# Kernel optimization log

Hardware: AMD Instinct MI355X
Metric: run time of the kernel (lower is better)

## Reference

```python
import jax, jax.numpy as jnp
import numpy as np

EPS = 1e-12
H = 256
W = 256
RANK = 4
CTX = 1024
BATCH = 32
FF = (H + W) * RANK * 4  # 8192
STD = 0.001


def _norm(x, axis):
    # torch: (x - mean) / sqrt(var(unbiased) + eps)
    m = jnp.mean(x, axis=axis, keepdims=True)
    v = jnp.var(x, axis=axis, keepdims=True, ddof=1)
    return (x - m) / jnp.sqrt(v + EPS)


def _norm_polar(x):
    # x: [B, N, 2]; magnitude-normalize relative to per-batch max magnitude
    x_abs = jnp.sqrt(x[..., 0] ** 2 + x[..., 1] ** 2 + EPS)          # [B, N]
    h = x_abs / (jnp.max(x_abs, axis=-1, keepdims=True) + EPS)       # [B, N]
    xn = x / (x_abs[..., None] + EPS)                                # [B, N, 2]
    return jnp.stack([h * xn[..., 0], h * xn[..., 1]], axis=-1)


def setup_inputs() -> dict:
    key = jax.random.key(0)
    ks = jax.random.split(key, 12)

    def lin(k, fan_in, shape):
        b = 1.0 / np.sqrt(fan_in)
        return jax.random.uniform(k, shape, jnp.float32, -b, b)

    weights_static = jnp.concatenate([
        jax.random.normal(ks[9], (1, H, W, 2), jnp.float32) * STD,
        jax.random.normal(ks[10], (1, H, W, 2), jnp.float32) * STD
        + jnp.array([1.0, 0.0], jnp.float32),
    ], axis=0)  # [2, H, W, 2]

    return {
        "x": jax.random.normal(ks[0], (BATCH, CTX), jnp.float32),
        "W_in": lin(ks[1], CTX, (FF, CTX)),
        "b_in": lin(ks[2], CTX, (FF,)),
        "W_gate": lin(ks[3], CTX, (FF, CTX)),
        "b_gate": lin(ks[4], CTX, (FF,)),
        "W_t": lin(ks[5], FF, (FF, FF)),
        "b_t": lin(ks[6], FF, (FF,)),
        "conv_w": lin(ks[7], RANK, (RANK, RANK)),  # 1x1 conv kernel [out, in]
        "conv_b": lin(ks[8], RANK, (RANK,)),
        "weights_static": weights_static,
        "weights_mod": jax.random.normal(ks[11], (4, H, W), jnp.float32) * STD,
    }


def reference(x, W_in, b_in, W_gate, b_gate, W_t, b_t, conv_w, conv_b,
              weights_static, weights_mod):
    b = x.shape[0]
    # dual linear projections (dropout p=0 -> identity)
    xt = x @ W_in.T + b_in            # [B, FF]
    xg = x @ W_gate.T + b_gate        # [B, FF]
    stack = jnp.stack([xt, xg], axis=0).reshape(2, b, 4, -1)
    stack = _norm(stack, -1)
    ctx = (stack[0] * jnp.tanh(stack[1])).reshape(b, -1)   # gated, [B, FF]
    ctx = ctx @ W_t.T + b_t                                 # [B, FF]
    ctx = ctx.reshape(b, 4, RANK, H + W)
    modc = _norm(ctx, -1)
    # outer product -> [B, 4, RANK, H, W]
    mod = jnp.tanh(jnp.einsum('bkri,bkrj->bkrij', modc[..., :H], modc[..., H:]))
    # channel 0: 1x1 conv over rank channels, then sum channels (keepdim)
    mod_real = jnp.einsum('oi,bihw->bohw', conv_w, mod[:, 0]) + conv_b[None, :, None, None]
    mod_real = jnp.sum(mod_real, axis=1, keepdims=True)     # [B, 1, H, W]
    mod_other = jnp.sum(mod[:, 1:], axis=2)                 # [B, 3, H, W]
    mod = jnp.concatenate([mod_real, mod_other], axis=1)    # [B, 4, H, W]
    mod = weights_mod[None] * mod

    A0 = weights_static[0]            # [H, W, 2]
    A1 = weights_static[1]            # [H, W, 2]
    Bm = jnp.moveaxis(mod[:, 0:2], 1, -1)                   # [B, H, W, 2]
    ms_r = A1[..., 0] * Bm[..., 0] - A1[..., 1] * Bm[..., 1]
    ms_i = A1[..., 0] * Bm[..., 1] - A1[..., 1] * Bm[..., 0]
    mod_scaled = jnp.stack([ms_r, ms_i], axis=-1)           # [B, H, W, 2]
    mod_scaled = _norm_polar(mod_scaled.reshape(b, H * W, 2)).reshape(b, H, W, 2)

    mag = jnp.sqrt(mod_scaled[..., 0] ** 2 + mod_scaled[..., 1] ** 2 + EPS)
    mag = jnp.sqrt(jnp.mean(mag, axis=(-1, -2)) + EPS)      # [B]
    mod_scaled = mod_scaled / mag[:, None, None, None]

    mod_weights = A0[None] + mod_scaled                     # [B, H, W, 2]

    mod_proj = jnp.moveaxis(mod[:, 2:], 1, -1)              # [B, H, W, 2]
    mod_proj = _norm_polar(mod_proj.reshape(b, H * W, 2)).reshape(b, H, W, 2)
    den = jnp.sqrt(mod_proj[..., 0] ** 2 + mod_proj[..., 1] ** 2 + EPS)
    theta_cos = mod_proj[..., 0] / den
    theta_sin = mod_proj[..., 1] / den
    weights = mod_weights[..., 0] * theta_cos + mod_weights[..., 1] * theta_sin
    return weights  # [B, H, W]
```

## Files before the change

### kernel.cpp

```cpp
#include <hip/hip_runtime.h>
#include <cstddef>

#define NB   32
#define CTXD 1024
#define FFD  8192
#define HD   256
#define WD   256
#define NPIX 65536
#define EPSF 1e-12f

typedef __attribute__((ext_vector_type(8))) short bf16x8;
typedef __attribute__((ext_vector_type(4))) float f32x4;


__device__ __forceinline__ float ftanh(float x){
  float ax = fabsf(x);
  float e  = __expf(2.0f*ax);
  float r  = 1.0f - 2.0f*__builtin_amdgcn_rcpf(e + 1.0f);
  return copysignf(r, x);
}

__device__ __forceinline__ unsigned short f2bf(float f){
  unsigned u = __float_as_uint(f);
  unsigned r = (u + 0x7FFFu + ((u >> 16) & 1u)) >> 16;
  return (unsigned short)r;
}
__device__ __forceinline__ float bf2f(unsigned short s){
  return __uint_as_float((unsigned)s << 16);
}

__device__ __forceinline__ void split3(float f, unsigned short& s0,
                                       unsigned short& s1, unsigned short& s2){
  s0 = f2bf(f);
  float r1 = f - bf2f(s0);
  s1 = f2bf(r1);
  float r2 = r1 - bf2f(s1);
  s2 = f2bf(r2);
}

__device__ __forceinline__ void gload_lds16(const void* g, void* l){
  __builtin_amdgcn_global_load_lds(
      (__attribute__((address_space(1))) void*)g,
      (__attribute__((address_space(3))) void*)l, 16, 0, 0);
}

__device__ __forceinline__ void block_reduce4(float& a, float& b, float& c, float& d){
  for (int off = 32; off > 0; off >>= 1){
    a += __shfl_down(a, off); b += __shfl_down(b, off);
    c += __shfl_down(c, off); d += __shfl_down(d, off);
  }
  __shared__ float lds[16];
  int wid = threadIdx.x >> 6, lane = threadIdx.x & 63;
  if (lane == 0){ lds[wid*4+0]=a; lds[wid*4+1]=b; lds[wid*4+2]=c; lds[wid*4+3]=d; }
  __syncthreads();
  a = (lds[0]+lds[4])+(lds[8]+lds[12]);
  b = (lds[1]+lds[5])+(lds[9]+lds[13]);
  c = (lds[2]+lds[6])+(lds[10]+lds[14]);
  d = (lds[3]+lds[7])+(lds[11]+lds[15]);
}

__device__ __forceinline__ void pixel_core(
    const float* __restrict__ lds, int h, int w, int pix,
    float cw0, float cw1, float cw2, float cw3, float cb,
    const float* __restrict__ wmod, const float* __restrict__ wstat,
    float& r_, float& i_, float& p_, float& q_){
  float sk[4];
  #pragma unroll
  for (int k = 0; k < 4; ++k){
    float acc = 0.f;
    #pragma unroll
    for (int r = 0; r < 4; ++r){
      int kr = k*4 + r;
      float u  = lds[kr*512 + h];
      float vv = lds[kr*512 + 256 + w];
      float tt = ftanh(u*vv);
      float cwr = (r==0)?cw0:(r==1)?cw1:(r==2)?cw2:cw3;
      acc += (k==0) ? cwr*tt : tt;
    }
    sk[k] = acc;
  }
  sk[0] += cb;
  float m0 = sk[0]*wmod[0*NPIX+pix];
  float m1 = sk[1]*wmod[1*NPIX+pix];
  float m2 = sk[2]*wmod[2*NPIX+pix];
  float m3 = sk[3]*wmod[3*NPIX+pix];
  float2 A1 = *(const float2*)(wstat + (size_t)(NPIX + pix)*2);
  r_ = A1.x*m0 - A1.y*m1;
  i_ = A1.x*m1 - A1.y*m0;
  p_ = m2; q_ = m3;
}


__global__ __launch_bounds__(256) void k_prep(
    const float* __restrict__ x, unsigned short* __restrict__ P,
    float* __restrict__ red){
  int g = blockIdx.x*256 + threadIdx.x;
  if (g < 64) red[g] = 0.0f;
  int b = g >> 7, grp = g & 127;
  int koff = grp*8;
  int c = grp >> 2, kg = grp & 3;
  const float* src = x + (size_t)b*CTXD + koff;
  float4 v0 = *(const float4*)(src), v1 = *(const float4*)(src+4);
  float vv[8] = {v0.x,v0.y,v0.z,v0.w,v1.x,v1.y,v1.z,v1.w};
  bf16x8 a0, a1, a2;
  #pragma unroll
  for (int e = 0; e < 8; ++e){
    unsigned short s0,s1,s2; split3(vv[e],s0,s1,s2);
    a0[e]=(short)s0; a1[e]=(short)s1; a2[e]=(short)s2;
  }
  size_t base = (size_t)c*3072 + (b>>4)*512 + kg*128 + (b&15)*8;
  *(bf16x8*)(P + base)        = a0;
  *(bf16x8*)(P + base + 1024) = a1;
  *(bf16x8*)(P + base + 2048) = a2;
}

__global__ __launch_bounds__(256) void k_gemm_reuse(
    const float* __restrict__ W0, const float* __restrict__ W1,
    const unsigned short* __restrict__ BP,
    float* __restrict__ Cp, int K, size_t zstride){
  __shared__ float wtile[2][4096];
  __shared__ unsigned short bpack[24576];
  const int t = threadIdx.x;
  const int wv = t >> 6, lane = t & 63;
  const int row = lane & 15, kg = lane >> 4;
  const int f0 = blockIdx.x * 128;
  const int kc = blockIdx.y;
  const float* __restrict__ W = blockIdx.z ? W1 : W0;
  const int kb = kc * 256;

  {
    const unsigned short* bsrc = BP + (size_t)(kc*8)*3072;
    #pragma unroll
    for (int i = 0; i < 12; ++i){
      int call = wv*12 + i;
      gload_lds16(bsrc + call*512 + lane*8, bpack + call*512);
    }
  }
  auto stageW = [&](int buf, int s){
    const int kbase = kb + s*32;
    #pragma unroll
    for (int i = 0; i < 4; ++i){
      int call = wv*4 + i;
      const float* src = W + (size_t)(f0 + call*8 + (lane>>3))*K + kbase
                           + (((lane&7) ^ ((lane>>3)&7)) << 2);
      gload_lds16(src, &wtile[buf][call*256]);
    }
  };

  stageW(0, 0);
  asm volatile("s_waitcnt vmcnt(0)" ::: "memory");
  __syncthreads();

  f32x4 acc0l={0.f,0.f,0.f,0.f}, acc0h={0.f,0.f,0.f,0.f};
  f32x4 acc1l={0.f,0.f,0.f,0.f}, acc1h={0.f,0.f,0.f,0.f};
  int cur = 0;
  const int sw = row & 7;

  for (int s = 0; s < 8; ++s){
    if (s + 1 < 8) stageW(cur ^ 1, s + 1);
    asm volatile("s_waitcnt vmcnt(4)" ::: "memory");
    __builtin_amdgcn_sched_barrier(0);
    const unsigned short* bch = bpack + s*3072 + kg*128 + row*8;
    bf16x8 b0 = *(const bf16x8*)(bch);
    bf16x8 b1 = *(const bf16x8*)(bch +  512);
    bf16x8 b2 = *(const bf16x8*)(bch + 1024);
    bf16x8 b3 = *(const bf16x8*)(bch + 1536);
    bf16x8 b4 = *(const bf16x8*)(bch + 2048);
    bf16x8 b5 = *(const bf16x8*)(bch + 2560);
    #pragma unroll
    for (int T = 0; T < 2; ++T){
      const float* wr = &wtile[cur][(wv*32 + T*16 + row)*32];
      float4 lo = *(const float4*)(wr + (((2*kg  ) ^ sw) << 2));
      float4 hi = *(const float4*)(wr + (((2*kg+1) ^ sw) << 2));
      bf16x8 a0, a1, a2;
      float wv8[8] = {lo.x,lo.y,lo.z,lo.w,hi.x,hi.y,hi.z,hi.w};
      #pragma unroll
      for (int e = 0; e < 8; ++e){
        unsigned short s0,s1,s2; split3(wv8[e],s0,s1,s2);
        a0[e]=(short)s0; a1[e]=(short)s1; a2[e]=(short)s2;
      }
      f32x4 al = T ? acc1l : acc0l, ah = T ? acc1h : acc0h;
      al = __builtin_amdgcn_mfma_f32_16x16x32_bf16(a0, b0, al, 0,0,0);
      ah = __builtin_amdgcn_mfma_f32_16x16x32_bf16(a0, b1, ah, 0,0,0);
      al = __builtin_amdgcn_mfma_f32_16x16x32_bf16(a0, b2, al, 0,0,0);
      ah = __builtin_amdgcn_mfma_f32_16x16x32_bf16(a0, b3, ah, 0,0,0);
      al = __builtin_amdgcn_mfma_f32_16x16x32_bf16(a1, b0, al, 0,0,0);
      ah = __builtin_amdgcn_mfma_f32_16x16x32_bf16(a1, b1, ah, 0,0,0);
      al = __builtin_amdgcn_mfma_f32_16x16x32_bf16(a0, b4, al, 0,0,0);
      ah = __builtin_amdgcn_mfma_f32_16x16x32_bf16(a0, b5, ah, 0,0,0);
      al = __builtin_amdgcn_mfma_f32_16x16x32_bf16(a1, b2, al, 0,0,0);
      ah = __builtin_amdgcn_mfma_f32_16x16x32_bf16(a1, b3, ah, 0,0,0);
      al = __builtin_amdgcn_mfma_f32_16x16x32_bf16(a2, b0, al, 0,0,0);
      ah = __builtin_amdgcn_mfma_f32_16x16x32_bf16(a2, b1, ah, 0,0,0);
      if (T){ acc1l = al; acc1h = ah; } else { acc0l = al; acc0h = ah; }
    }
    cur ^= 1;
  }

  float* __restrict__ C = Cp + (size_t)blockIdx.z*zstride + (size_t)kc*(FFD*32);
  #pragma unroll
  for (int r = 0; r < 4; ++r){
    int fA = f0 + wv*32 + kg*4 + r;
    int fB = fA + 16;
    C[(size_t)fA*32 + row]      = acc0l[r];
    C[(size_t)fA*32 + 16 + row] = acc0h[r];
    C[(size_t)fB*32 + row]      = acc1l[r];
    C[(size_t)fB*32 + 16 + row] = acc1h[r];
  }
}

__global__ __launch_bounds__(256) void k_reduce1(
    const float* __restrict__ Cp, const float* __restrict__ bin,
    const float* __restrict__ bg, float* __restrict__ xtT,
    float* __restrict__ xgT){
  int g = blockIdx.x*256 + threadIdx.x;
  int m = g >> 18, idx = g & 262143;
  int f = idx >> 5;
  const float* __restrict__ cp = Cp + (size_t)m*(4ull*FFD*32);
  float s = (m ? bg : bin)[f];
  #pragma unroll
  for (int sI = 0; sI < 4; ++sI) s += cp[(size_t)sI*(FFD*32) + idx];
  (m ? xgT : xtT)[idx] = s;
}

__global__ __launch_bounds__(256) void k_reduce2(
    const float* __restrict__ Cp, const float* __restrict__ bias,
    float* __restrict__ outT){
  int g = blockIdx.x*256 + threadIdx.x;
  int f = g >> 5;
  float s = bias[f];
  #pragma unroll
  for (int sI = 0; sI < 32; ++sI) s += Cp[(size_t)sI*(FFD*32) + g];
  outT[g] = s;
}

__global__ __launch_bounds__(256) void k_normgate(
    const float* __restrict__ xtT, const float* __restrict__ xgT,
    unsigned short* __restrict__ P){
  int b = blockIdx.x >> 2, g4 = blockIdx.x & 3;
  int t = threadIdx.x;
  int f8 = g4*2048 + t*8;
  float vt[8], vg[8];
  float st=0.f, sst=0.f, sg=0.f, ssg=0.f;
  #pragma unroll
  for (int i = 0; i < 8; ++i){
    int f = f8 + i;
    float a = xtT[(size_t)f*NB + b];
    float c = xgT[(size_t)f*NB + b];
    vt[i]=a; vg[i]=c;
    st += a; sst += a*a; sg += c; ssg += c*c;
  }
  block_reduce4(st, sst, sg, ssg);
  float mt = st * (1.0f/2048.0f);
  float it = rsqrtf((sst - st*mt) * (1.0f/2047.0f) + EPSF);
  float mg = sg * (1.0f/2048.0f);
  float ig = rsqrtf((ssg - sg*mg) * (1.0f/2047.0f) + EPSF);
  bf16x8 a0, a1, a2;
  #pragma unroll
  for (int i = 0; i < 8; ++i){
    float nt = (vt[i]-mt)*it;
    float ng = (vg[i]-mg)*ig;
    float cv = nt * ftanh(ng);
    unsigned short s0,s1,s2; split3(cv,s0,s1,s2);
    a0[i]=(short)s0; a1[i]=(short)s1; a2[i]=(short)s2;
  }
  int c2 = f8 >> 5, kg = (f8 >> 3) & 3;
  size_t base = (size_t)c2*3072 + (b>>4)*512 + kg*128 + (b&15)*8;
  *(bf16x8*)(P + base)        = a0;
  *(bf16x8*)(P + base + 1024) = a1;
  *(bf16x8*)(P + base + 2048) = a2;
}

__global__ __launch_bounds__(256) void k_norm512(
    const float* __restrict__ ctx2T, float* __restrict__ modc){
  int b = blockIdx.x >> 4, kr = blockIdx.x & 15;
  int t = threadIdx.x;
  int base = kr*512;
  float v0 = ctx2T[(base + t      )*NB + b];
  float v1 = ctx2T[(base + 256 + t)*NB + b];
  float s = v0+v1, ss = v0*v0 + v1*v1, d0=0.f, d1=0.f;
  block_reduce4(s, ss, d0, d1);
  float m   = s * (1.0f/512.0f);
  float inv = rsqrtf((ss - s*m) * (1.0f/511.0f) + EPSF);
  modc[b*FFD + base + t      ] = (v0-m)*inv;
  modc[b*FFD + base + 256 + t] = (v1-m)*inv;
}

__global__ __launch_bounds__(256) void k_scan(
    const float* __restrict__ modc,
    const float* __restrict__ convw, const float* __restrict__ convb,
    const float* __restrict__ wmod, const float* __restrict__ wstat,
    float* __restrict__ red, float* __restrict__ magpart){
  int b = blockIdx.x >> 4, chunk = blockIdx.x & 15;
  int t = threadIdx.x;
  __shared__ float lds[16*512];
  #pragma unroll
  for (int i = 0; i < 8; ++i){
    float4 v = *(const float4*)(modc + (size_t)b*FFD + (i*256 + t)*4);
    *(float4*)(lds + (i*256 + t)*4) = v;
  }
  float cw0 = convw[0]+convw[4]+convw[8]+convw[12];
  float cw1 = convw[1]+convw[5]+convw[9]+convw[13];
  float cw2 = convw[2]+convw[6]+convw[10]+convw[14];
  float cw3 = convw[3]+convw[7]+convw[11]+convw[15];
  float cb  = convb[0]+convb[1]+convb[2]+convb[3];
  __syncthreads();
  int w = t;
  float mxs = 0.f, mxp = 0.f, sas = 0.f;
  for (int it = 0; it < 16; ++it){
    int h = chunk*16 + it;
    int pix = h*WD + w;
    float r_, i_, p_, q_;
    pixel_core(lds, h, w, pix, cw0, cw1, cw2, cw3, cb, wmod, wstat,
               r_, i_, p_, q_);
    float as = sqrtf(r_*r_ + i_*i_ + EPSF);
    float ap = sqrtf(p_*p_ + q_*q_ + EPSF);
    mxs = fmaxf(mxs, as); mxp = fmaxf(mxp, ap);
    sas += as;
  }
  for (int off = 32; off > 0; off >>= 1){
    mxs = fmaxf(mxs, __shfl_down(mxs, off));
    mxp = fmaxf(mxp, __shfl_down(mxp, off));
    sas += __shfl_down(sas, off);
  }
  __shared__ float lred[12];
  int wid = t >> 6, lane = t & 63;
  if (lane == 0){ lred[wid] = mxs; lred[4+wid] = mxp; lred[8+wid] = sas; }
  __syncthreads();
  if (t == 0){
    float a = fmaxf(fmaxf(lred[0],lred[1]), fmaxf(lred[2],lred[3]));
    float p = fmaxf(fmaxf(lred[4],lred[5]), fmaxf(lred[6],lred[7]));
    float s = (lred[8]+lred[9])+(lred[10]+lred[11]);
    atomicMax((int*)&red[b],    __float_as_int(a));
    atomicMax((int*)&red[32+b], __float_as_int(p));
    magpart[b*16 + chunk] = s;
  }
}

__global__ __launch_bounds__(256) void k_final(
    const float* __restrict__ modc,
    const float* __restrict__ convw, const float* __restrict__ convb,
    const float* __restrict__ wmod, const float* __restrict__ wstat,
    const float* __restrict__ red, const float* __restrict__ magpart,
    float* __restrict__ out){
  int b = blockIdx.x >> 4, chunk = blockIdx.x & 15;
  int t = threadIdx.x;
  __shared__ float lds[16*512];
  __shared__ float s_im;
  if (t < 16){
    float v = magpart[b*16 + t];
    for (int off = 8; off > 0; off >>= 1) v += __shfl_down(v, off);
    if (t == 0){
      float maxs = red[b];
      s_im = rsqrtf(v*(1.0f/65536.0f)/(maxs + EPSF) + EPSF);
    }
  }
  #pragma unroll
  for (int i = 0; i < 8; ++i){
    float4 v = *(const float4*)(modc + (size_t)b*FFD + (i*256 + t)*4);
    *(float4*)(lds + (i*256 + t)*4) = v;
  }
  float cw0 = convw[0]+convw[4]+convw[8]+convw[12];
  float cw1 = convw[1]+convw[5]+convw[9]+convw[13];
  float cw2 = convw[2]+convw[6]+convw[10]+convw[14];
  float cw3 = convw[3]+convw[7]+convw[11]+convw[15];
  float cb  = convb[0]+convb[1]+convb[2]+convb[3];
  __syncthreads();
  float im = s_im;
  float maxs = red[b], maxp = red[32+b];
  int w = t;
  for (int it = 0; it < 16; ++it){
    int h = chunk*16 + it;
    int pix = h*WD + w;
    float r_, i_, p_, q_;
    pixel_core(lds, h, w, pix, cw0, cw1, cw2, cw3, cb, wmod, wstat,
               r_, i_, p_, q_);
    float as = sqrtf(r_*r_ + i_*i_ + EPSF);
    float fs = (as/(maxs+EPSF))/(as+EPSF)*im;
    float2 A0 = *(const float2*)(wstat + (size_t)pix*2);
    float mwr = A0.x + fs*r_;
    float mwi = A0.y + fs*i_;
    float ap = sqrtf(p_*p_ + q_*q_ + EPSF);
    float fp = (ap/(maxp+EPSF))/(ap+EPSF);
    float mpr = fp*p_, mpi = fp*q_;
    float den = sqrtf(mpr*mpr + mpi*mpi + EPSF);
    out[(size_t)b*NPIX + pix] = (mwr*mpr + mwi*mpi)/den;
  }
}


extern "C" void kernel_launch(void* const* d_in, const int* in_sizes, int n_in,
                              void* d_out, int out_size, void* d_ws, size_t ws_size,
                              hipStream_t stream){
  const float* x     = (const float*)d_in[0];
  const float* Win   = (const float*)d_in[1];
  const float* bin   = (const float*)d_in[2];
  const float* Wg    = (const float*)d_in[3];
  const float* bg    = (const float*)d_in[4];
  const float* Wt    = (const float*)d_in[5];
  const float* bt    = (const float*)d_in[6];
  const float* convw = (const float*)d_in[7];
  const float* convb = (const float*)d_in[8];
  const float* wstat = (const float*)d_in[9];
  const float* wmod  = (const float*)d_in[10];
  float* out = (float*)d_out;
  float* ws  = (float*)d_ws;

  float* xtT   = ws;
  float* xgT   = ws + 262144;
  float* ctx2T = ws;
  float* modc  = ws + 262144;
  unsigned short* P2 = (unsigned short*)(ws + 524288);
  unsigned short* P1 = (unsigned short*)(ws + 917504);
  float* Cp    = ws + 966656;
  float* red     = ws + 9355264;
  float* magpart = ws + 9355328;

  k_prep<<<16, 256, 0, stream>>>(x, P1, red);
  k_gemm_reuse<<<dim3(64,4,2), 256, 0, stream>>>(Win, Wg, P1,
                                                 Cp, CTXD, 4ull*FFD*32);
  k_reduce1<<<2048, 256, 0, stream>>>(Cp, bin, bg, xtT, xgT);
  k_normgate<<<128, 256, 0, stream>>>(xtT, xgT, P2);
  k_gemm_reuse<<<dim3(64,32,1), 256, 0, stream>>>(Wt, Wt, P2,
                                                  Cp, FFD, 0);
  k_reduce2<<<1024, 256, 0, stream>>>(Cp, bt, ctx2T);
  k_norm512<<<512, 256, 0, stream>>>(ctx2T, modc);
  k_scan<<<512, 256, 0, stream>>>(modc, convw, convb, wmod, wstat, red, magpart);
  k_final<<<512, 256, 0, stream>>>(modc, convw, convb, wmod, wstat, red,
                                   magpart, out);
}
```

Before: 160.7 us.

## Use scaled fp16 two-term split MFMA and fuse split-K reductions into norms

Replaces the three-term bf16 splitting of both GEMM operands with a two-term fp16 split, where the residual is scaled by 4096. This cuts the MFMA count per step from 12 to 6 and shrinks the packed B buffer and its LDS footprint. The two accumulator sets are combined at store time. The separate split-K reduction kernels are removed, and the partial sums are added directly inside the normalization kernels, saving two launches and an intermediate round-trip. The risks are lower precision from fp16's narrower range, and strided, uncoalesced partial-sum reads inside the norm kernels.

```diff
diff --git a/kernel.cpp b/kernel.cpp
--- a/kernel.cpp
+++ b/kernel.cpp
@@ -8,8 +8,10 @@
 #define WD   256
 #define NPIX 65536
 #define EPSF 1e-12f
-
-typedef __attribute__((ext_vector_type(8))) short bf16x8;
+#define SCF  4096.0f
+#define ISCF (1.0f/4096.0f)
+
+typedef __attribute__((ext_vector_type(8))) _Float16 half8;
 typedef __attribute__((ext_vector_type(4))) float f32x4;
 
 
@@ -20,22 +22,10 @@
   return copysignf(r, x);
 }
 
-__device__ __forceinline__ unsigned short f2bf(float f){
-  unsigned u = __float_as_uint(f);
-  unsigned r = (u + 0x7FFFu + ((u >> 16) & 1u)) >> 16;
-  return (unsigned short)r;
-}
-__device__ __forceinline__ float bf2f(unsigned short s){
-  return __uint_as_float((unsigned)s << 16);
-}
-
-__device__ __forceinline__ void split3(float f, unsigned short& s0,
-                                       unsigned short& s1, unsigned short& s2){
-  s0 = f2bf(f);
-  float r1 = f - bf2f(s0);
-  s1 = f2bf(r1);
-  float r2 = r1 - bf2f(s1);
-  s2 = f2bf(r2);
+__device__ __forceinline__ void split2h(float f, _Float16& h0, _Float16& h1){
+  h0 = (_Float16)f;
+  float r = (f - (float)h0) * SCF;
+  h1 = (_Float16)r;
 }
 
 __device__ __forceinline__ void gload_lds16(const void* g, void* l){
@@ -97,21 +87,19 @@
   int g = blockIdx.x*256 + threadIdx.x;
   if (g < 64) red[g] = 0.0f;
   int b = g >> 7, grp = g & 127;
-  int koff = grp*8;
   int c = grp >> 2, kg = grp & 3;
-  const float* src = x + (size_t)b*CTXD + koff;
+  const float* src = x + (size_t)b*CTXD + grp*8;
   float4 v0 = *(const float4*)(src), v1 = *(const float4*)(src+4);
   float vv[8] = {v0.x,v0.y,v0.z,v0.w,v1.x,v1.y,v1.z,v1.w};
-  bf16x8 a0, a1, a2;
+  half8 g0, g1;
   #pragma unroll
   for (int e = 0; e < 8; ++e){
-    unsigned short s0,s1,s2; split3(vv[e],s0,s1,s2);
-    a0[e]=(short)s0; a1[e]=(short)s1; a2[e]=(short)s2;
-  }
-  size_t base = (size_t)c*3072 + (b>>4)*512 + kg*128 + (b&15)*8;
-  *(bf16x8*)(P + base)        = a0;
-  *(bf16x8*)(P + base + 1024) = a1;
-  *(bf16x8*)(P + base + 2048) = a2;
+    _Float16 h0,h1; split2h(vv[e],h0,h1);
+    g0[e]=h0; g1[e]=h1;
+  }
+  size_t base = (size_t)c*2048 + (b>>4)*512 + kg*128 + (b&15)*8;
+  *(half8*)(P + base)        = g0;
+  *(half8*)(P + base + 1024) = g1;
 }
 
 __global__ __launch_bounds__(256) void k_gemm_reuse(
@@ -119,7 +107,7 @@
     const unsigned short* __restrict__ BP,
     float* __restrict__ Cp, int K, size_t zstride){
   __shared__ float wtile[2][4096];
-  __shared__ unsigned short bpack[24576];
+  __shared__ unsigned short bpack[16384];
   const int t = threadIdx.x;
   const int wv = t >> 6, lane = t & 63;
   const int row = lane & 15, kg = lane >> 4;
@@ -129,10 +117,10 @@
   const int kb = kc * 256;
 
   {
-    const unsigned short* bsrc = BP + (size_t)(kc*8)*3072;
-    #pragma unroll
-    for (int i = 0; i < 12; ++i){
-      int call = wv*12 + i;
+    const unsigned short* bsrc = BP + (size_t)(kc*8)*2048;
+    #pragma unroll
+    for (int i = 0; i < 8; ++i){
+      int call = wv*8 + i;
       gload_lds16(bsrc + call*512 + lane*8, bpack + call*512);
     }
   }
@@ -151,8 +139,10 @@
   asm volatile("s_waitcnt vmcnt(0)" ::: "memory");
   __syncthreads();
 
-  f32x4 acc0l={0.f,0.f,0.f,0.f}, acc0h={0.f,0.f,0.f,0.f};
-  f32x4 acc1l={0.f,0.f,0.f,0.f}, acc1h={0.f,0.f,0.f,0.f};
+  f32x4 aH0l={0.f,0.f,0.f,0.f}, aH0h={0.f,0.f,0.f,0.f};
+  f32x4 aL0l={0.f,0.f,0.f,0.f}, aL0h={0.f,0.f,0.f,0.f};
+  f32x4 aH1l={0.f,0.f,0.f,0.f}, aH1h={0.f,0.f,0.f,0.f};
+  f32x4 aL1l={0.f,0.f,0.f,0.f}, aL1h={0.f,0.f,0.f,0.f};
   int cur = 0;
   const int sw = row & 7;
 
@@ -160,39 +150,38 @@
     if (s + 1 < 8) stageW(cur ^ 1, s + 1);
     asm volatile("s_waitcnt vmcnt(4)" ::: "memory");
     __builtin_amdgcn_sched_barrier(0);
-    const unsigned short* bch = bpack + s*3072 + kg*128 + row*8;
-    bf16x8 b0 = *(const bf16x8*)(bch);
-    bf16x8 b1 = *(const bf16x8*)(bch +  512);
-    bf16x8 b2 = *(const bf16x8*)(bch + 1024);
-    bf16x8 b3 = *(const bf16x8*)(bch + 1536);
-    bf16x8 b4 = *(const bf16x8*)(bch + 2048);
-    bf16x8 b5 = *(const bf16x8*)(bch + 2560);
+    const unsigned short* bch = bpack + s*2048 + kg*128 + row*8;
+    half8 b0l = *(const half8*)(bch);
+    half8 b0h = *(const half8*)(bch +  512);
+    half8 b1l = *(const half8*)(bch + 1024);
+    half8 b1h = *(const half8*)(bch + 1536);
     #pragma unroll
     for (int T = 0; T < 2; ++T){
       const float* wr = &wtile[cur][(wv*32 + T*16 + row)*32];
       float4 lo = *(const float4*)(wr + (((2*kg  ) ^ sw) << 2));
       float4 hi = *(const float4*)(wr + (((2*kg+1) ^ sw) << 2));
-      bf16x8 a0, a1, a2;
+      half8 a0, a1;
       float wv8[8] = {lo.x,lo.y,lo.z,lo.w,hi.x,hi.y,hi.z,hi.w};
       #pragma unroll
       for (int e = 0; e < 8; ++e){
-        unsigned short s0,s1,s2; split3(wv8[e],s0,s1,s2);
-        a0[e]=(short)s0; a1[e]=(short)s1; a2[e]=(short)s2;
+        _Float16 h0,h1; split2h(wv8[e],h0,h1);
+        a0[e]=h0; a1[e]=h1;
       }
-      f32x4 al = T ? acc1l : acc0l, ah = T ? acc1h : acc0h;
-      al = __builtin_amdgcn_mfma_f32_16x16x32_bf16(a0, b0, al, 0,0,0);
-      ah = __builtin_amdgcn_mfma_f32_16x16x32_bf16(a0, b1, ah, 0,0,0);
-      al = __builtin_amdgcn_mfma_f32_16x16x32_bf16(a0, b2, al, 0,0,0);
-      ah = __builtin_amdgcn_mfma_f32_16x16x32_bf16(a0, b3, ah, 0,0,0);
-      al = __builtin_amdgcn_mfma_f32_16x16x32_bf16(a1, b0, al, 0,0,0);
-      ah = __builtin_amdgcn_mfma_f32_16x16x32_bf16(a1, b1, ah, 0,0,0);
-      al = __builtin_amdgcn_mfma_f32_16x16x32_bf16(a0, b4, al, 0,0,0);
-      ah = __builtin_amdgcn_mfma_f32_16x16x32_bf16(a0, b5, ah, 0,0,0);
-      al = __builtin_amdgcn_mfma_f32_16x16x32_bf16(a1, b2, al, 0,0,0);
-      ah = __builtin_amdgcn_mfma_f32_16x16x32_bf16(a1, b3, ah, 0,0,0);
-      al = __builtin_amdgcn_mfma_f32_16x16x32_bf16(a2, b0, al, 0,0,0);
-      ah = __builtin_amdgcn_mfma_f32_16x16x32_bf16(a2, b1, ah, 0,0,0);
-      if (T){ acc1l = al; acc1h = ah; } else { acc0l = al; acc0h = ah; }
+      if (T == 0){
+        aH0l = __builtin_amdgcn_mfma_f32_16x16x32_f16(a0, b0l, aH0l, 0,0,0);
+        aH0h = __builtin_amdgcn_mfma_f32_16x16x32_f16(a0, b0h, aH0h, 0,0,0);
+        aL0l = __builtin_amdgcn_mfma_f32_16x16x32_f16(a0, b1l, aL0l, 0,0,0);
+        aL0h = __builtin_amdgcn_mfma_f32_16x16x32_f16(a0, b1h, aL0h, 0,0,0);
+        aL0l = __builtin_amdgcn_mfma_f32_16x16x32_f16(a1, b0l, aL0l, 0,0,0);
+        aL0h = __builtin_amdgcn_mfma_f32_16x16x32_f16(a1, b0h, aL0h, 0,0,0);
+      } else {
+        aH1l = __builtin_amdgcn_mfma_f32_16x16x32_f16(a0, b0l, aH1l, 0,0,0);
+        aH1h = __builtin_amdgcn_mfma_f32_16x16x32_f16(a0, b0h, aH1h, 0,0,0);
+        aL1l = __builtin_amdgcn_mfma_f32_16x16x32_f16(a0, b1l, aL1l, 0,0,0);
+        aL1h = __builtin_amdgcn_mfma_f32_16x16x32_f16(a0, b1h, aL1h, 0,0,0);
+        aL1l = __builtin_amdgcn_mfma_f32_16x16x32_f16(a1, b0l, aL1l, 0,0,0);
+        aL1h = __builtin_amdgcn_mfma_f32_16x16x32_f16(a1, b0h, aL1h, 0,0,0);
+      }
     }
     cur ^= 1;
   }
@@ -202,41 +191,16 @@
   for (int r = 0; r < 4; ++r){
     int fA = f0 + wv*32 + kg*4 + r;
     int fB = fA + 16;
-    C[(size_t)fA*32 + row]      = acc0l[r];
-    C[(size_t)fA*32 + 16 + row] = acc0h[r];
-    C[(size_t)fB*32 + row]      = acc1l[r];
-    C[(size_t)fB*32 + 16 + row] = acc1h[r];
-  }
-}
-
-__global__ __launch_bounds__(256) void k_reduce1(
+    C[(size_t)fA*32 + row]      = aH0l[r] + aL0l[r]*ISCF;
+    C[(size_t)fA*32 + 16 + row] = aH0h[r] + aL0h[r]*ISCF;
+    C[(size_t)fB*32 + row]      = aH1l[r] + aL1l[r]*ISCF;
+    C[(size_t)fB*32 + 16 + row] = aH1h[r] + aL1h[r]*ISCF;
+  }
+}
+
+__global__ __launch_bounds__(256) void k_norm1(
     const float* __restrict__ Cp, const float* __restrict__ bin,
-    const float* __restrict__ bg, float* __restrict__ xtT,
-    float* __restrict__ xgT){
-  int g = blockIdx.x*256 + threadIdx.x;
-  int m = g >> 18, idx = g & 262143;
-  int f = idx >> 5;
-  const float* __restrict__ cp = Cp + (size_t)m*(4ull*FFD*32);
-  float s = (m ? bg : bin)[f];
-  #pragma unroll
-  for (int sI = 0; sI < 4; ++sI) s += cp[(size_t)sI*(FFD*32) + idx];
-  (m ? xgT : xtT)[idx] = s;
-}
-
-__global__ __launch_bounds__(256) void k_reduce2(
-    const float* __restrict__ Cp, const float* __restrict__ bias,
-    float* __restrict__ outT){
-  int g = blockIdx.x*256 + threadIdx.x;
-  int f = g >> 5;
-  float s = bias[f];
-  #pragma unroll
-  for (int sI = 0; sI < 32; ++sI) s += Cp[(size_t)sI*(FFD*32) + g];
-  outT[g] = s;
-}
-
-__global__ __launch_bounds__(256) void k_normgate(
-    const float* __restrict__ xtT, const float* __restrict__ xgT,
-    unsigned short* __restrict__ P){
+    const float* __restrict__ bg, unsigned short* __restrict__ P){
   int b = blockIdx.x >> 2, g4 = blockIdx.x & 3;
   int t = threadIdx.x;
   int f8 = g4*2048 + t*8;
@@ -245,8 +209,12 @@
   #pragma unroll
   for (int i = 0; i < 8; ++i){
     int f = f8 + i;
-    float a = xtT[(size_t)f*NB + b];
-    float c = xgT[(size_t)f*NB + b];
+    float a = bin[f], c = bg[f];
+    #pragma unroll
+    for (int kc = 0; kc < 4; ++kc){
+      a += Cp[((size_t)kc*FFD + f)*32 + b];
+      c += Cp[((size_t)(4+kc)*FFD + f)*32 + b];
+    }
     vt[i]=a; vg[i]=c;
     st += a; sst += a*a; sg += c; ssg += c*c;
   }
@@ -255,35 +223,40 @@
   float it = rsqrtf((sst - st*mt) * (1.0f/2047.0f) + EPSF);
   float mg = sg * (1.0f/2048.0f);
   float ig = rsqrtf((ssg - sg*mg) * (1.0f/2047.0f) + EPSF);
-  bf16x8 a0, a1, a2;
+  half8 g0, g1;
   #pragma unroll
   for (int i = 0; i < 8; ++i){
     float nt = (vt[i]-mt)*it;
     float ng = (vg[i]-mg)*ig;
     float cv = nt * ftanh(ng);
-    unsigned short s0,s1,s2; split3(cv,s0,s1,s2);
-    a0[i]=(short)s0; a1[i]=(short)s1; a2[i]=(short)s2;
+    _Float16 h0,h1; split2h(cv,h0,h1);
+    g0[i]=h0; g1[i]=h1;
   }
   int c2 = f8 >> 5, kg = (f8 >> 3) & 3;
-  size_t base = (size_t)c2*3072 + (b>>4)*512 + kg*128 + (b&15)*8;
-  *(bf16x8*)(P + base)        = a0;
-  *(bf16x8*)(P + base + 1024) = a1;
-  *(bf16x8*)(P + base + 2048) = a2;
-}
-
-__global__ __launch_bounds__(256) void k_norm512(
-    const float* __restrict__ ctx2T, float* __restrict__ modc){
+  size_t base = (size_t)c2*2048 + (b>>4)*512 + kg*128 + (b&15)*8;
+  *(half8*)(P + base)        = g0;
+  *(half8*)(P + base + 1024) = g1;
+}
+
+__global__ __launch_bounds__(256) void k_norm2(
+    const float* __restrict__ Cp, const float* __restrict__ bt,
+    float* __restrict__ modc){
   int b = blockIdx.x >> 4, kr = blockIdx.x & 15;
   int t = threadIdx.x;
   int base = kr*512;
-  float v0 = ctx2T[(base + t      )*NB + b];
-  float v1 = ctx2T[(base + 256 + t)*NB + b];
+  int fa = base + t, fb = base + 256 + t;
+  float v0 = bt[fa], v1 = bt[fb];
+  #pragma unroll
+  for (int s = 0; s < 32; ++s){
+    v0 += Cp[((size_t)s*FFD + fa)*32 + b];
+    v1 += Cp[((size_t)s*FFD + fb)*32 + b];
+  }
   float s = v0+v1, ss = v0*v0 + v1*v1, d0=0.f, d1=0.f;
   block_reduce4(s, ss, d0, d1);
   float m   = s * (1.0f/512.0f);
   float inv = rsqrtf((ss - s*m) * (1.0f/511.0f) + EPSF);
-  modc[b*FFD + base + t      ] = (v0-m)*inv;
-  modc[b*FFD + base + 256 + t] = (v1-m)*inv;
+  modc[b*FFD + fa] = (v0-m)*inv;
+  modc[b*FFD + fb] = (v1-m)*inv;
 }
 
 __global__ __launch_bounds__(256) void k_scan(
@@ -406,9 +379,6 @@
   float* out = (float*)d_out;
   float* ws  = (float*)d_ws;
 
-  float* xtT   = ws;
-  float* xgT   = ws + 262144;
-  float* ctx2T = ws;
   float* modc  = ws + 262144;
   unsigned short* P2 = (unsigned short*)(ws + 524288);
   unsigned short* P1 = (unsigned short*)(ws + 917504);
@@ -419,12 +389,10 @@
   k_prep<<<16, 256, 0, stream>>>(x, P1, red);
   k_gemm_reuse<<<dim3(64,4,2), 256, 0, stream>>>(Win, Wg, P1,
                                                  Cp, CTXD, 4ull*FFD*32);
-  k_reduce1<<<2048, 256, 0, stream>>>(Cp, bin, bg, xtT, xgT);
-  k_normgate<<<128, 256, 0, stream>>>(xtT, xgT, P2);
+  k_norm1<<<128, 256, 0, stream>>>(Cp, bin, bg, P2);
   k_gemm_reuse<<<dim3(64,32,1), 256, 0, stream>>>(Wt, Wt, P2,
                                                   Cp, FFD, 0);
-  k_reduce2<<<1024, 256, 0, stream>>>(Cp, bt, ctx2T);
-  k_norm512<<<512, 256, 0, stream>>>(ctx2T, modc);
+  k_norm2<<<512, 256, 0, stream>>>(Cp, bt, modc);
   k_scan<<<512, 256, 0, stream>>>(modc, convw, convb, wmod, wstat, red, magpart);
   k_final<<<512, 256, 0, stream>>>(modc, convw, convb, wmod, wstat, red,
                                    magpart, out);
```

Result: slower. 181.0 us (+12.7%).
